# Kernel optimization log

Measured on AMD Instinct MI355X. Metric: run time of the kernel, lower is better.

## Reference

```python
import jax, jax.numpy as jnp
import numpy as np

E = 8      # num_experts
D = 1024   # input_size
H = 1024   # hidden_size
K = 2      # top_k
B = 2
S = 1024


def setup_inputs() -> dict:
    key = jax.random.key(0)
    ks = jax.random.split(key, 5)
    x = jax.random.normal(ks[0], (B, S, D), dtype=jnp.float32)
    p = jax.random.uniform(ks[1], (B * S, K), dtype=jnp.float32)
    expert_p = p / p.sum(axis=-1, keepdims=True)            # normalized top-k gates
    expert_idxs = jax.random.randint(ks[2], (B * S, K), 0, E)
    W1 = jax.random.normal(ks[3], (E, D, 2 * H), dtype=jnp.float32) * (D ** -0.5)
    W2 = jax.random.normal(ks[4], (E, H, D), dtype=jnp.float32) * (H ** -0.5)
    return {"x": x, "expert_p": expert_p, "expert_idxs": expert_idxs, "W1": W1, "W2": W2}


def reference(x, expert_p, expert_idxs, W1, W2):
    x_shape = x.shape
    xf = x.reshape(-1, x_shape[-1])                 # [N, D]
    n_tok = xf.shape[0]
    k = expert_idxs.shape[-1]
    x_pair = jnp.repeat(xf, k, axis=0)              # [N*K, D] token replicated per expert slot
    idx = expert_idxs.reshape(-1)                   # [N*K]
    p = expert_p.reshape(-1)                        # [N*K]
    y_pair = jnp.zeros((n_tok * k, x_shape[-1]), dtype=x.dtype)
    # loop over fixed small expert count; masked dense GEMM per expert
    for e in range(W1.shape[0]):
        m = (idx == e).astype(x.dtype)[:, None]     # [N*K, 1]
        hg = (x_pair * m) @ W1[e]                   # [N*K, 2H]
        h, g = jnp.split(hg, 2, axis=-1)            # chunk(2): (h, gates)
        a = jax.nn.silu(g) * h                      # SiLU-gated GLU
        y_pair = y_pair + (a @ W2[e]) * m           # [N*K, D]
    # combine: weight each pair by its gate prob and sum over top_k slots
    y = (y_pair * p[:, None]).reshape(n_tok, k, -1).sum(axis=1)
    return y.reshape(x_shape)
```

## Files before the change

kernel.cpp:

```cpp
#include <hip/hip_runtime.h>


typedef __bf16 bf16x8 __attribute__((ext_vector_type(8)));
typedef __bf16 bf16x4 __attribute__((ext_vector_type(4)));
typedef float  f32x4  __attribute__((ext_vector_type(4)));

#define NPAIR 4096
#define NTOK  2048
#define DDIM  1024
#define HDIM  1024
#define NEXP  8

#define ORDER_I   64
#define XB_OFF    (24576)
#define W1T_OFF   (XB_OFF + 4194304)
#define W2T_OFF   (W1T_OFF + 33554432)
#define ACT_OFF   (W2T_OFF + 16777216)

#define GLOAD_LDS16(g, l) \
    __builtin_amdgcn_global_load_lds( \
        (const __attribute__((address_space(1))) void*)(g), \
        (__attribute__((address_space(3))) void*)(l), 16, 0, 0)

__device__ __forceinline__ void tcvt2(const float* __restrict__ s,
                                      __bf16* __restrict__ d,
                                      int R, int C, int k0, int c0,
                                      float* tt, int tid) {
#pragma unroll
    for (int j = 0; j < 8; j++) {
        int c = j * 256 + tid;
        int row = c >> 5, col = (c & 31) * 4;
        GLOAD_LDS16(s + (size_t)(k0 + row) * C + c0 + col, (char*)tt + c * 16);
    }
    __syncthreads();
    const int a = tid >> 5, b = tid & 31;
    f32x4 v[8];
#pragma unroll
    for (int jj = 0; jj < 8; jj++)
        v[jj] = *(const f32x4*)(tt + (8 * a + jj) * 128 + 4 * b);
#pragma unroll
    for (int ii = 0; ii < 4; ii++) {
        bf16x8 o;
#pragma unroll
        for (int jj = 0; jj < 8; jj++) o[jj] = (__bf16)v[jj][ii];
        *(bf16x8*)(d + (size_t)(c0 + 4 * b + ii) * R + k0 + 8 * a) = o;
    }
}

__global__ __launch_bounds__(256) void prep_kernel(const float* __restrict__ x,
                                                   const float* __restrict__ W1,
                                                   const int* __restrict__ idx,
                                                   int* __restrict__ wsi,
                                                   __bf16* __restrict__ xb,
                                                   __bf16* __restrict__ w1t,
                                                   float* __restrict__ out) {
    __shared__ __align__(16) float tt[64 * 128];
    __shared__ int cnt[NEXP];
    __shared__ int sbase, scur;
    const int b = blockIdx.x;
    const int tid = threadIdx.x;
    if (b < 2048) {
        int e = b >> 8, t2 = b & 255;
        int k0 = (t2 & 15) * 64, c0 = (t2 >> 4) * 128;
        tcvt2(W1 + (size_t)e * DDIM * 2 * HDIM, w1t + (size_t)e * 2 * HDIM * DDIM,
              DDIM, 2 * HDIM, k0, c0, tt, tid);
    } else if (b < 2304) {
        size_t base = (size_t)(b - 2048) * 8192 + tid * 8;
#pragma unroll
        for (int j = 0; j < 4; j++) {
            const float* sp = x + base + j * 2048;
            f32x4 v0 = *(const f32x4*)sp;
            f32x4 v1 = *(const f32x4*)(sp + 4);
            bf16x8 o;
            o[0] = (__bf16)v0[0]; o[1] = (__bf16)v0[1]; o[2] = (__bf16)v0[2]; o[3] = (__bf16)v0[3];
            o[4] = (__bf16)v1[0]; o[5] = (__bf16)v1[1]; o[6] = (__bf16)v1[2]; o[7] = (__bf16)v1[3];
            *(bf16x8*)(xb + base + j * 2048) = o;
        }
    } else if (b < 2816) {
        int zb = b - 2304;
        float4 z4 = {0.f, 0.f, 0.f, 0.f};
        int b4 = zb * 4096;
#pragma unroll
        for (int j = 0; j < 4; j++)
            *(float4*)(out + b4 + j * 1024 + tid * 4) = z4;
    } else {
        const int e = b - 2816;
        if (tid < NEXP) cnt[tid] = 0;
        if (tid == 0) scur = 0;
        __syncthreads();
        for (int i = tid; i < NPAIR; i += 256) atomicAdd(&cnt[idx[i] & 7], 1);
        __syncthreads();
        if (tid == 0) {
            int off = 0;
            for (int e2 = 0; e2 < NEXP; e2++) {
                if (e2 == e) { wsi[e] = cnt[e]; wsi[8 + e] = off; sbase = off; }
                off += (cnt[e2] + 127) & ~127;
            }
        }
        __syncthreads();
        for (int i = tid; i < NPAIR; i += 256) {
            if ((idx[i] & 7) == e) {
                int s = atomicAdd(&scur, 1);
                wsi[ORDER_I + sbase + s] = i;
            }
        }
    }
}

__global__ __launch_bounds__(256) void gemm1_kernel(const __bf16* __restrict__ xb,
                                                    const __bf16* __restrict__ w1t,
                                                    const int* __restrict__ wsi,
                                                    __bf16* __restrict__ act,
                                                    const float* __restrict__ W2,
                                                    __bf16* __restrict__ w2t) {
    __shared__ __align__(16) char smem[49152];
    const int tid = threadIdx.x;
    const int z = blockIdx.z;

    if (z >= 8) {
        int aux = blockIdx.y * 16 + blockIdx.x;
        int e = aux >> 7, t2 = aux & 127;
        int k0 = (t2 & 15) * 64, c0 = (t2 >> 4) * 128;
        tcvt2(W2 + (size_t)e * HDIM * DDIM, w2t + (size_t)e * DDIM * HDIM,
              HDIM, DDIM, k0, c0, (float*)smem, tid);
        return;
    }

    const int e = z;
    const int cnt = wsi[e];
    const int m0 = blockIdx.y * 64;
    if (m0 >= cnt) return;
    const int base = wsi[8 + e];
    const int n0 = blockIdx.x * 64;
    const int* order = wsi + ORDER_I;
    const __bf16* w1e = w1t + (size_t)e * 2048 * 1024;

    const int lane = tid & 63, w = tid >> 6;
    const int lm = lane & 15, q = lane >> 4;
    const int wm = w & 1, wn = w >> 1;
    const int x7 = lm & 7;
    const int sw0 = (q ^ x7) * 16;
    const int sw1 = ((4 + q) ^ x7) * 16;

    const __bf16* ga[2];
    const __bf16* gb[4];
#pragma unroll
    for (int j = 0; j < 2; j++) {
        int c = j * 256 + tid;
        int r = c >> 3;
        int ks = ((c & 7) ^ (r & 7)) * 8;
        int m = m0 + r; if (m >= cnt) m = cnt - 1;
        int tok = order[base + m] >> 1;
        ga[j] = xb + (size_t)tok * DDIM + ks;
    }
#pragma unroll
    for (int j = 0; j < 4; j++) {
        int c = j * 256 + tid;
        int r = c >> 3;
        int ks = ((c & 7) ^ (r & 7)) * 8;
        int half = r >> 6, rr = r & 63;
        int rb = (rr < 32) ? (n0 + half * 32 + rr)
                           : (HDIM + n0 + half * 32 + (rr - 32));
        gb[j] = w1e + (size_t)rb * DDIM + ks;
    }

    f32x4 acc[2][4];
#pragma unroll
    for (int mt = 0; mt < 2; mt++)
#pragma unroll
        for (int nt = 0; nt < 4; nt++) acc[mt][nt] = (f32x4){0.f, 0.f, 0.f, 0.f};

#pragma unroll
    for (int j = 0; j < 2; j++) {
        GLOAD_LDS16(ga[j], smem + (j * 256 + tid) * 16);
        ga[j] += 64;
    }
#pragma unroll
    for (int j = 0; j < 4; j++) {
        GLOAD_LDS16(gb[j], smem + 8192 + (j * 256 + tid) * 16);
        gb[j] += 64;
    }

    for (int t = 0; t < 16; ++t) {
        char* cbase = smem + (t & 1) * 24576;
        if (t < 15) {
            char* nbase = smem + ((t + 1) & 1) * 24576;
#pragma unroll
            for (int j = 0; j < 2; j++) {
                GLOAD_LDS16(ga[j], nbase + (j * 256 + tid) * 16);
                ga[j] += 64;
            }
#pragma unroll
            for (int j = 0; j < 4; j++) {
                GLOAD_LDS16(gb[j], nbase + 8192 + (j * 256 + tid) * 16);
                gb[j] += 64;
            }
            asm volatile("s_waitcnt vmcnt(6)" ::: "memory");
        } else {
            asm volatile("s_waitcnt vmcnt(0)" ::: "memory");
        }
        __builtin_amdgcn_s_barrier();
        __builtin_amdgcn_sched_barrier(0);
        __bf16 (*As)[64] = (__bf16 (*)[64])cbase;
        __bf16 (*Bs)[64] = (__bf16 (*)[64])(cbase + 8192);
#pragma unroll
        for (int kh = 0; kh < 2; kh++) {
            const int sw = kh ? sw1 : sw0;
            bf16x8 af[2];
#pragma unroll
            for (int mt = 0; mt < 2; mt++)
                af[mt] = *(const bf16x8*)((const char*)&As[wm * 32 + mt * 16 + lm][0] + sw);
            __builtin_amdgcn_s_setprio(1);
#pragma unroll
            for (int nt = 0; nt < 4; nt++) {
                bf16x8 bfr = *(const bf16x8*)((const char*)&Bs[wn * 64 + nt * 16 + lm][0] + sw);
#pragma unroll
                for (int mt = 0; mt < 2; mt++)
                    acc[mt][nt] = __builtin_amdgcn_mfma_f32_16x16x32_bf16(af[mt], bfr, acc[mt][nt], 0, 0, 0);
            }
            __builtin_amdgcn_s_setprio(0);
        }
        __builtin_amdgcn_sched_barrier(0);
        __builtin_amdgcn_s_barrier();
    }

#pragma unroll
    for (int mt = 0; mt < 2; mt++) {
        int mbase = m0 + wm * 32 + mt * 16 + q * 4;
#pragma unroll
        for (int ntp = 0; ntp < 2; ntp++) {
            int col = n0 + wn * 32 + ntp * 16 + lm;
#pragma unroll
            for (int r = 0; r < 4; r++) {
                int m = mbase + r;
                if (m < cnt) {
                    float h = acc[mt][ntp][r];
                    float g = acc[mt][ntp + 2][r];
                    float a = h * (g / (1.f + __expf(-g)));
                    act[(size_t)(base + m) * HDIM + col] = (__bf16)a;
                }
            }
        }
    }
}

__global__ __launch_bounds__(256) void gemm2_kernel(const __bf16* __restrict__ act,
                                                    const __bf16* __restrict__ w2t,
                                                    const int* __restrict__ wsi,
                                                    const float* __restrict__ p,
                                                    float* __restrict__ out) {
    const int e = blockIdx.z;
    const int cnt = wsi[e];
    const int m0 = blockIdx.y * 64;
    if (m0 >= cnt) return;
    const int base = wsi[8 + e];
    const int n0 = blockIdx.x * 64;
    const int* order = wsi + ORDER_I;
    const __bf16* w2e = w2t + (size_t)e * 1024 * 1024;

    __shared__ __align__(16) char smem[49152];

    const int tid = threadIdx.x;
    const int lane = tid & 63, w = tid >> 6;
    const int lm = lane & 15, q = lane >> 4;
    const int wm = w & 1, wn = w >> 1;
    const int x7 = lm & 7;
    const int sw0 = (q ^ x7) * 16;
    const int sw1 = ((4 + q) ^ x7) * 16;

    const __bf16* ga[2];
    const __bf16* gb[2];
#pragma unroll
    for (int j = 0; j < 2; j++) {
        int c = j * 256 + tid;
        int r = c >> 3;
        int ks = ((c & 7) ^ (r & 7)) * 8;
        ga[j] = act + (size_t)(base + m0 + r) * HDIM + ks;
        gb[j] = w2e + (size_t)(n0 + r) * HDIM + ks;
    }

    f32x4 acc[2][2];
#pragma unroll
    for (int mt = 0; mt < 2; mt++)
#pragma unroll
        for (int nt = 0; nt < 2; nt++) acc[mt][nt] = (f32x4){0.f, 0.f, 0.f, 0.f};

#pragma unroll
    for (int t = 0; t < 2; ++t) {
        char* nb = smem + t * 16384;
#pragma unroll
        for (int j = 0; j < 2; j++) {
            GLOAD_LDS16(ga[j], nb + (j * 256 + tid) * 16);
            GLOAD_LDS16(gb[j], nb + 8192 + (j * 256 + tid) * 16);
            ga[j] += 64; gb[j] += 64;
        }
    }

    for (int t = 0; t < 16; ++t) {
        char* cbase = smem + (t % 3) * 16384;
        if (t < 14) {
            char* nbase = smem + ((t + 2) % 3) * 16384;
#pragma unroll
            for (int j = 0; j < 2; j++) {
                GLOAD_LDS16(ga[j], nbase + (j * 256 + tid) * 16);
                GLOAD_LDS16(gb[j], nbase + 8192 + (j * 256 + tid) * 16);
                ga[j] += 64; gb[j] += 64;
            }
            asm volatile("s_waitcnt vmcnt(8)" ::: "memory");
        } else if (t == 14) {
            asm volatile("s_waitcnt vmcnt(4)" ::: "memory");
        } else {
            asm volatile("s_waitcnt vmcnt(0)" ::: "memory");
        }
        __builtin_amdgcn_s_barrier();
        __builtin_amdgcn_sched_barrier(0);
        __bf16 (*As)[64] = (__bf16 (*)[64])cbase;
        __bf16 (*Bs)[64] = (__bf16 (*)[64])(cbase + 8192);
#pragma unroll
        for (int kh = 0; kh < 2; kh++) {
            const int sw = kh ? sw1 : sw0;
            bf16x8 af[2];
#pragma unroll
            for (int mt = 0; mt < 2; mt++)
                af[mt] = *(const bf16x8*)((const char*)&As[wm * 32 + mt * 16 + lm][0] + sw);
            __builtin_amdgcn_s_setprio(1);
#pragma unroll
            for (int nt = 0; nt < 2; nt++) {
                bf16x8 bfr = *(const bf16x8*)((const char*)&Bs[wn * 32 + nt * 16 + lm][0] + sw);
#pragma unroll
                for (int mt = 0; mt < 2; mt++)
                    acc[mt][nt] = __builtin_amdgcn_mfma_f32_16x16x32_bf16(af[mt], bfr, acc[mt][nt], 0, 0, 0);
            }
            __builtin_amdgcn_s_setprio(0);
        }
        __builtin_amdgcn_sched_barrier(0);
        __builtin_amdgcn_s_barrier();
    }

    int pi[2][4];
    float pw[2][4];
#pragma unroll
    for (int mt = 0; mt < 2; mt++)
#pragma unroll
        for (int r = 0; r < 4; r++) {
            int gm = m0 + wm * 32 + mt * 16 + q * 4 + r;
            if (gm < cnt) {
                int pr = order[base + gm];
                pi[mt][r] = pr;
                pw[mt][r] = p[pr];
            } else pi[mt][r] = -1;
        }
#pragma unroll
    for (int mt = 0; mt < 2; mt++)
#pragma unroll
        for (int nt = 0; nt < 2; nt++) {
            int col = n0 + wn * 32 + nt * 16 + lm;
#pragma unroll
            for (int r = 0; r < 4; r++) {
                if (pi[mt][r] >= 0) {
                    int tok = pi[mt][r] >> 1;
                    atomicAdd(out + (size_t)tok * DDIM + col, pw[mt][r] * acc[mt][nt][r]);
                }
            }
        }
}

extern "C" void kernel_launch(void* const* d_in, const int* in_sizes, int n_in,
                              void* d_out, int out_size, void* d_ws, size_t ws_size,
                              hipStream_t stream) {
    (void)in_sizes; (void)n_in; (void)out_size; (void)ws_size;
    const float* x   = (const float*)d_in[0];
    const float* p   = (const float*)d_in[1];
    const int* eidx  = (const int*)d_in[2];
    const float* W1  = (const float*)d_in[3];
    const float* W2  = (const float*)d_in[4];
    float* out = (float*)d_out;

    char* ws = (char*)d_ws;
    int* wsi     = (int*)ws;
    __bf16* xb   = (__bf16*)(ws + XB_OFF);
    __bf16* w1t  = (__bf16*)(ws + W1T_OFF);
    __bf16* w2t  = (__bf16*)(ws + W2T_OFF);
    __bf16* act  = (__bf16*)(ws + ACT_OFF);

    prep_kernel<<<2824, 256, 0, stream>>>(x, W1, eidx, wsi, xb, w1t, out);
    gemm1_kernel<<<dim3(16, 64, 9), 256, 0, stream>>>(xb, w1t, wsi, act, W2, w2t);
    gemm2_kernel<<<dim3(16, 64, NEXP), 256, 0, stream>>>(act, w2t, wsi, p, out);
}
```

Measured before the change: 205.5 us.

## Enlarge GEMM M-tile to 128 rows with per-wave M split in both MoE GEMMs

Both expert GEMMs now use 128-row M tiles, with each of the four waves owning 32 rows across the full 64-column N tile. The grid's M dimension is halved to match. This raises reuse of the W1/W2 weight tiles and halves the number of blocks that re-read weights. gemm1 keeps separate h and gate accumulators, and its W2 transpose blocks now handle two tiles each. gemm2 drops its triple buffer for a double buffer, and LDS rises to 64KB in gemm1, which may reduce occupancy and weaken latency hiding. Blocks also become coarser for the ragged per-expert counts (~512 rows each).

```diff
diff --git a/kernel.cpp b/kernel.cpp
--- a/kernel.cpp
+++ b/kernel.cpp
@@ -113,22 +113,27 @@
                                                     __bf16* __restrict__ act,
                                                     const float* __restrict__ W2,
                                                     __bf16* __restrict__ w2t) {
-    __shared__ __align__(16) char smem[49152];
+    __shared__ __align__(16) char smem[65536];
     const int tid = threadIdx.x;
     const int z = blockIdx.z;
 
     if (z >= 8) {
         int aux = blockIdx.y * 16 + blockIdx.x;
-        int e = aux >> 7, t2 = aux & 127;
-        int k0 = (t2 & 15) * 64, c0 = (t2 >> 4) * 128;
-        tcvt2(W2 + (size_t)e * HDIM * DDIM, w2t + (size_t)e * DDIM * HDIM,
-              HDIM, DDIM, k0, c0, (float*)smem, tid);
+#pragma unroll
+        for (int tt2 = 0; tt2 < 2; tt2++) {
+            int tile = aux * 2 + tt2;
+            int e = tile >> 7, t2 = tile & 127;
+            int k0 = (t2 & 15) * 64, c0 = (t2 >> 4) * 128;
+            tcvt2(W2 + (size_t)e * HDIM * DDIM, w2t + (size_t)e * DDIM * HDIM,
+                  HDIM, DDIM, k0, c0, (float*)smem, tid);
+            if (tt2 == 0) __syncthreads();
+        }
         return;
     }
 
     const int e = z;
     const int cnt = wsi[e];
-    const int m0 = blockIdx.y * 64;
+    const int m0 = blockIdx.y * 128;
     if (m0 >= cnt) return;
     const int base = wsi[8 + e];
     const int n0 = blockIdx.x * 64;
@@ -137,15 +142,15 @@
 
     const int lane = tid & 63, w = tid >> 6;
     const int lm = lane & 15, q = lane >> 4;
-    const int wm = w & 1, wn = w >> 1;
+    const int wm = w;
     const int x7 = lm & 7;
     const int sw0 = (q ^ x7) * 16;
     const int sw1 = ((4 + q) ^ x7) * 16;
 
-    const __bf16* ga[2];
+    const __bf16* ga[4];
     const __bf16* gb[4];
 #pragma unroll
-    for (int j = 0; j < 2; j++) {
+    for (int j = 0; j < 4; j++) {
         int c = j * 256 + tid;
         int r = c >> 3;
         int ks = ((c & 7) ^ (r & 7)) * 8;
@@ -164,45 +169,48 @@
         gb[j] = w1e + (size_t)rb * DDIM + ks;
     }
 
-    f32x4 acc[2][4];
+    f32x4 acch[2][4], accg[2][4];
 #pragma unroll
     for (int mt = 0; mt < 2; mt++)
 #pragma unroll
-        for (int nt = 0; nt < 4; nt++) acc[mt][nt] = (f32x4){0.f, 0.f, 0.f, 0.f};
-
-#pragma unroll
-    for (int j = 0; j < 2; j++) {
+        for (int c = 0; c < 4; c++) {
+            acch[mt][c] = (f32x4){0.f, 0.f, 0.f, 0.f};
+            accg[mt][c] = (f32x4){0.f, 0.f, 0.f, 0.f};
+        }
+
+#pragma unroll
+    for (int j = 0; j < 4; j++) {
         GLOAD_LDS16(ga[j], smem + (j * 256 + tid) * 16);
         ga[j] += 64;
     }
 #pragma unroll
     for (int j = 0; j < 4; j++) {
-        GLOAD_LDS16(gb[j], smem + 8192 + (j * 256 + tid) * 16);
+        GLOAD_LDS16(gb[j], smem + 16384 + (j * 256 + tid) * 16);
         gb[j] += 64;
     }
 
     for (int t = 0; t < 16; ++t) {
-        char* cbase = smem + (t & 1) * 24576;
+        char* cbase = smem + (t & 1) * 32768;
         if (t < 15) {
-            char* nbase = smem + ((t + 1) & 1) * 24576;
-#pragma unroll
-            for (int j = 0; j < 2; j++) {
+            char* nbase = smem + ((t + 1) & 1) * 32768;
+#pragma unroll
+            for (int j = 0; j < 4; j++) {
                 GLOAD_LDS16(ga[j], nbase + (j * 256 + tid) * 16);
                 ga[j] += 64;
             }
 #pragma unroll
             for (int j = 0; j < 4; j++) {
-                GLOAD_LDS16(gb[j], nbase + 8192 + (j * 256 + tid) * 16);
+                GLOAD_LDS16(gb[j], nbase + 16384 + (j * 256 + tid) * 16);
                 gb[j] += 64;
             }
-            asm volatile("s_waitcnt vmcnt(6)" ::: "memory");
+            asm volatile("s_waitcnt vmcnt(8)" ::: "memory");
         } else {
             asm volatile("s_waitcnt vmcnt(0)" ::: "memory");
         }
         __builtin_amdgcn_s_barrier();
         __builtin_amdgcn_sched_barrier(0);
         __bf16 (*As)[64] = (__bf16 (*)[64])cbase;
-        __bf16 (*Bs)[64] = (__bf16 (*)[64])(cbase + 8192);
+        __bf16 (*Bs)[64] = (__bf16 (*)[64])(cbase + 16384);
 #pragma unroll
         for (int kh = 0; kh < 2; kh++) {
             const int sw = kh ? sw1 : sw0;
@@ -212,11 +220,15 @@
                 af[mt] = *(const bf16x8*)((const char*)&As[wm * 32 + mt * 16 + lm][0] + sw);
             __builtin_amdgcn_s_setprio(1);
 #pragma unroll
-            for (int nt = 0; nt < 4; nt++) {
-                bf16x8 bfr = *(const bf16x8*)((const char*)&Bs[wn * 64 + nt * 16 + lm][0] + sw);
-#pragma unroll
-                for (int mt = 0; mt < 2; mt++)
-                    acc[mt][nt] = __builtin_amdgcn_mfma_f32_16x16x32_bf16(af[mt], bfr, acc[mt][nt], 0, 0, 0);
+            for (int c = 0; c < 4; c++) {
+                int hrow = (c >> 1) * 64 + (c & 1) * 16;
+                bf16x8 bh = *(const bf16x8*)((const char*)&Bs[hrow + lm][0] + sw);
+                bf16x8 bg = *(const bf16x8*)((const char*)&Bs[hrow + 32 + lm][0] + sw);
+#pragma unroll
+                for (int mt = 0; mt < 2; mt++) {
+                    acch[mt][c] = __builtin_amdgcn_mfma_f32_16x16x32_bf16(af[mt], bh, acch[mt][c], 0, 0, 0);
+                    accg[mt][c] = __builtin_amdgcn_mfma_f32_16x16x32_bf16(af[mt], bg, accg[mt][c], 0, 0, 0);
+                }
             }
             __builtin_amdgcn_s_setprio(0);
         }
@@ -228,14 +240,14 @@
     for (int mt = 0; mt < 2; mt++) {
         int mbase = m0 + wm * 32 + mt * 16 + q * 4;
 #pragma unroll
-        for (int ntp = 0; ntp < 2; ntp++) {
-            int col = n0 + wn * 32 + ntp * 16 + lm;
+        for (int c = 0; c < 4; c++) {
+            int col = n0 + c * 16 + lm;
 #pragma unroll
             for (int r = 0; r < 4; r++) {
                 int m = mbase + r;
                 if (m < cnt) {
-                    float h = acc[mt][ntp][r];
-                    float g = acc[mt][ntp + 2][r];
+                    float h = acch[mt][c][r];
+                    float g = accg[mt][c][r];
                     float a = h * (g / (1.f + __expf(-g)));
                     act[(size_t)(base + m) * HDIM + col] = (__bf16)a;
                 }
@@ -251,7 +263,7 @@
                                                     float* __restrict__ out) {
     const int e = blockIdx.z;
     const int cnt = wsi[e];
-    const int m0 = blockIdx.y * 64;
+    const int m0 = blockIdx.y * 128;
     if (m0 >= cnt) return;
     const int base = wsi[8 + e];
     const int n0 = blockIdx.x * 64;
@@ -263,59 +275,67 @@
     const int tid = threadIdx.x;
     const int lane = tid & 63, w = tid >> 6;
     const int lm = lane & 15, q = lane >> 4;
-    const int wm = w & 1, wn = w >> 1;
+    const int wm = w;
     const int x7 = lm & 7;
     const int sw0 = (q ^ x7) * 16;
     const int sw1 = ((4 + q) ^ x7) * 16;
 
-    const __bf16* ga[2];
+    const __bf16* ga[4];
     const __bf16* gb[2];
+#pragma unroll
+    for (int j = 0; j < 4; j++) {
+        int c = j * 256 + tid;
+        int r = c >> 3;
+        int ks = ((c & 7) ^ (r & 7)) * 8;
+        ga[j] = act + (size_t)(base + m0 + r) * HDIM + ks;
+    }
 #pragma unroll
     for (int j = 0; j < 2; j++) {
         int c = j * 256 + tid;
         int r = c >> 3;
         int ks = ((c & 7) ^ (r & 7)) * 8;
-        ga[j] = act + (size_t)(base + m0 + r) * HDIM + ks;
         gb[j] = w2e + (size_t)(n0 + r) * HDIM + ks;
     }
 
-    f32x4 acc[2][2];
+    f32x4 acc[2][4];
 #pragma unroll
     for (int mt = 0; mt < 2; mt++)
 #pragma unroll
-        for (int nt = 0; nt < 2; nt++) acc[mt][nt] = (f32x4){0.f, 0.f, 0.f, 0.f};
-
-#pragma unroll
-    for (int t = 0; t < 2; ++t) {
-        char* nb = smem + t * 16384;
-#pragma unroll
-        for (int j = 0; j < 2; j++) {
-            GLOAD_LDS16(ga[j], nb + (j * 256 + tid) * 16);
-            GLOAD_LDS16(gb[j], nb + 8192 + (j * 256 + tid) * 16);
-            ga[j] += 64; gb[j] += 64;
-        }
+        for (int nt = 0; nt < 4; nt++) acc[mt][nt] = (f32x4){0.f, 0.f, 0.f, 0.f};
+
+#pragma unroll
+    for (int j = 0; j < 4; j++) {
+        GLOAD_LDS16(ga[j], smem + (j * 256 + tid) * 16);
+        ga[j] += 64;
+    }
+#pragma unroll
+    for (int j = 0; j < 2; j++) {
+        GLOAD_LDS16(gb[j], smem + 16384 + (j * 256 + tid) * 16);
+        gb[j] += 64;
     }
 
     for (int t = 0; t < 16; ++t) {
-        char* cbase = smem + (t % 3) * 16384;
-        if (t < 14) {
-            char* nbase = smem + ((t + 2) % 3) * 16384;
+        char* cbase = smem + (t & 1) * 24576;
+        if (t < 15) {
+            char* nbase = smem + ((t + 1) & 1) * 24576;
+#pragma unroll
+            for (int j = 0; j < 4; j++) {
+                GLOAD_LDS16(ga[j], nbase + (j * 256 + tid) * 16);
+                ga[j] += 64;
+            }
 #pragma unroll
             for (int j = 0; j < 2; j++) {
-                GLOAD_LDS16(ga[j], nbase + (j * 256 + tid) * 16);
-                GLOAD_LDS16(gb[j], nbase + 8192 + (j * 256 + tid) * 16);
-                ga[j] += 64; gb[j] += 64;
-            }
-            asm volatile("s_waitcnt vmcnt(8)" ::: "memory");
-        } else if (t == 14) {
-            asm volatile("s_waitcnt vmcnt(4)" ::: "memory");
+                GLOAD_LDS16(gb[j], nbase + 16384 + (j * 256 + tid) * 16);
+                gb[j] += 64;
+            }
+            asm volatile("s_waitcnt vmcnt(6)" ::: "memory");
         } else {
             asm volatile("s_waitcnt vmcnt(0)" ::: "memory");
         }
         __builtin_amdgcn_s_barrier();
         __builtin_amdgcn_sched_barrier(0);
         __bf16 (*As)[64] = (__bf16 (*)[64])cbase;
-        __bf16 (*Bs)[64] = (__bf16 (*)[64])(cbase + 8192);
+        __bf16 (*Bs)[64] = (__bf16 (*)[64])(cbase + 16384);
 #pragma unroll
         for (int kh = 0; kh < 2; kh++) {
             const int sw = kh ? sw1 : sw0;
@@ -325,8 +345,8 @@
                 af[mt] = *(const bf16x8*)((const char*)&As[wm * 32 + mt * 16 + lm][0] + sw);
             __builtin_amdgcn_s_setprio(1);
 #pragma unroll
-            for (int nt = 0; nt < 2; nt++) {
-                bf16x8 bfr = *(const bf16x8*)((const char*)&Bs[wn * 32 + nt * 16 + lm][0] + sw);
+            for (int nt = 0; nt < 4; nt++) {
+                bf16x8 bfr = *(const bf16x8*)((const char*)&Bs[nt * 16 + lm][0] + sw);
 #pragma unroll
                 for (int mt = 0; mt < 2; mt++)
                     acc[mt][nt] = __builtin_amdgcn_mfma_f32_16x16x32_bf16(af[mt], bfr, acc[mt][nt], 0, 0, 0);
@@ -353,8 +373,8 @@
 #pragma unroll
     for (int mt = 0; mt < 2; mt++)
 #pragma unroll
-        for (int nt = 0; nt < 2; nt++) {
-            int col = n0 + wn * 32 + nt * 16 + lm;
+        for (int nt = 0; nt < 4; nt++) {
+            int col = n0 + nt * 16 + lm;
 #pragma unroll
             for (int r = 0; r < 4; r++) {
                 if (pi[mt][r] >= 0) {
@@ -384,6 +404,6 @@
     __bf16* act  = (__bf16*)(ws + ACT_OFF);
 
     prep_kernel<<<2824, 256, 0, stream>>>(x, W1, eidx, wsi, xb, w1t, out);
-    gemm1_kernel<<<dim3(16, 64, 9), 256, 0, stream>>>(xb, w1t, wsi, act, W2, w2t);
-    gemm2_kernel<<<dim3(16, 64, NEXP), 256, 0, stream>>>(act, w2t, wsi, p, out);
+    gemm1_kernel<<<dim3(16, 32, 9), 256, 0, stream>>>(xb, w1t, wsi, act, W2, w2t);
+    gemm2_kernel<<<dim3(16, 32, NEXP), 256, 0, stream>>>(act, w2t, wsi, p, out);
 }
```

After: 215.8 us. 1.05x slower.
